# Kernel optimization log

Measured on AMD Instinct MI355X. Metric: run time of the kernel, lower is better.

Reference implementation:

```python
import jax, jax.numpy as jnp
import numpy as np
from jax import lax

B, T, DIN = 512, 96, 64
H = 256          # hidden_dim
P = 2            # patch_size
L = 4            # n_layers
HEADS = 8
E = 3 * H        # encoder_dim = hidden_dim * len(scales)
NC = 100         # num_classes
EPS = 1e-5


def layernorm(x, g, b):
    m = x.mean(-1, keepdims=True)
    v = ((x - m) ** 2).mean(-1, keepdims=True)
    return (x - m) * lax.rsqrt(v + EPS) * g + b


def conv1d(x, w, b, k):
    # x: [B, C, T], w: [O, I, k]; torch padding='same' (extra pad on the right for even k)
    lo = (k - 1) // 2
    hi = (k - 1) - lo
    y = lax.conv_general_dilated(x, w, (1,), [(lo, hi)],
                                 dimension_numbers=('NCH', 'OIH', 'NCH'))
    return y + b[None, :, None]


def fourier_attn(x, Wqkv, Wo, bo):
    Bx, Tx, Ex = x.shape
    dh = Ex // HEADS
    qkv = x @ Wqkv                                   # [B,T,3E]
    q, k, v = jnp.split(qkv, 3, axis=-1)
    to_heads = lambda t: t.reshape(Bx, Tx, HEADS, dh).transpose(0, 2, 1, 3)  # [B,h,T,dh]
    q, k, v = to_heads(q), to_heads(k), to_heads(v)
    qf = jnp.fft.rfft(q, axis=-2)
    kf = jnp.fft.rfft(k, axis=-2)
    attn = jnp.sum(jnp.conj(qf) * kf, axis=-1).real * (dh ** -0.5)  # [B,h,F]
    attn = jax.nn.softmax(attn, axis=-1)
    vf = jnp.fft.rfft(v, axis=-2)                    # [B,h,F,dh]
    out = jnp.fft.irfft(attn[..., None] * vf, n=Tx, axis=-2)        # [B,h,T,dh]
    out = out.transpose(0, 2, 1, 3).reshape(Bx, Tx, Ex)
    return out @ Wo + bo


def setup_inputs() -> dict:
    key = jax.random.key(0)
    ks = iter(jax.random.split(key, 40))
    nrm = lambda shape, s=0.02: jax.random.normal(next(ks), shape, jnp.float32) * s
    z = lambda *shape: jnp.zeros(shape, jnp.float32)
    o = lambda *shape: jnp.ones(shape, jnp.float32)
    return dict(
        x=jax.random.normal(next(ks), (B, T, DIN), jnp.float32),
        W_in=nrm((DIN, H)), b_in=z(H),
        pe=nrm((1, 100, H)),
        W_shape=nrm((H, H)), b_shape=z(H),
        W_patch=nrm((P * H, H)), b_patch=z(H),
        conv_w1=nrm((H, H, 1)), conv_b1=z(H),
        conv_w2=nrm((H, H, 2)), conv_b2=z(H),
        conv_w4=nrm((H, H, 4)), conv_b4=z(H),
        ln1_g=o(L, E), ln1_b=z(L, E),
        Wqkv=nrm((L, E, 3 * E)),
        Wo=nrm((L, E, E)), bo=z(L, E),
        ln2_g=o(L, E), ln2_b=z(L, E),
        Wf1=nrm((L, E, 4 * E)), bf1=z(L, 4 * E),
        Wf2=nrm((L, 4 * E, E)), bf2=z(L, E),
        ssm_w=nrm((E, E, 3)), ssm_b=z(E),
        ssm_g=o(E), ssm_bn=z(E),
        W_out=nrm((E, NC)), b_out=z(NC),
    )


def reference(x, W_in, b_in, pe, W_shape, b_shape, W_patch, b_patch,
              conv_w1, conv_b1, conv_w2, conv_b2, conv_w4, conv_b4,
              ln1_g, ln1_b, Wqkv, Wo, bo, ln2_g, ln2_b, Wf1, bf1, Wf2, bf2,
              ssm_w, ssm_b, ssm_g, ssm_bn, W_out, b_out):
    h = x @ W_in + b_in                              # [B,T,H]
    h = h + pe[:, :h.shape[1], :]
    # shape-aware embedding: diff with prepend of first step
    sf = jnp.diff(h, axis=1, prepend=h[:, :1, :])
    h = h + sf @ W_shape + b_shape
    # patch embedding: [B,T,H] -> [B,T/P,P*H] -> [B,T/P,H]
    Bx, Tx, Dx = h.shape
    h = h.reshape(Bx, Tx // P, P * Dx) @ W_patch + b_patch
    # multiscale fourier: rfft.real then 3 same-padded convs, concat channels
    f = jnp.fft.rfft(h, axis=1).real                 # [B,F,H], F = T/P//2 + 1
    fc = f.transpose(0, 2, 1)                        # [B,H,F]
    m1 = conv1d(fc, conv_w1, conv_b1, 1).transpose(0, 2, 1)
    m2 = conv1d(fc, conv_w2, conv_b2, 2).transpose(0, 2, 1)
    m4 = conv1d(fc, conv_w4, conv_b4, 4).transpose(0, 2, 1)
    h = jnp.concatenate([m1, m2, m4], axis=-1)       # [B,F,E]
    for i in range(L):
        h = h + fourier_attn(layernorm(h, ln1_g[i], ln1_b[i]), Wqkv[i], Wo[i], bo[i])
        y = layernorm(h, ln2_g[i], ln2_b[i])
        y = jax.nn.gelu(y @ Wf1[i] + bf1[i], approximate=False) @ Wf2[i] + bf2[i]
        h = h + y
    # simple SSM: depth conv residual + layernorm
    s = conv1d(h.transpose(0, 2, 1), ssm_w, ssm_b, 3).transpose(0, 2, 1)
    h = layernorm(h + s, ssm_g, ssm_bn)
    return h.mean(axis=1) @ W_out + b_out            # [B,NC]
```

## Files before the change

### kernel.cpp

```cpp
#include <hip/hip_runtime.h>
#include <hip/hip_bf16.h>
#include <math.h>

#define Bsz 512
#define Tin 96
#define DIN 64
#define Hd  256
#define Pp  2
#define Ll  4
#define NHEAD 8
#define Ed  768
#define NCls 100
#define Tp  48
#define Ff  25
#define F2  13
#define DH  96

#define E_BIAS 1
#define E_PE   2
#define E_RES  4
#define E_ACC  8
#define E_GELU 16
#define E_OUTS 32
#define E_SPLK 64

typedef unsigned short ushortT;
typedef unsigned short ushort8 __attribute__((ext_vector_type(8)));
typedef short short8 __attribute__((ext_vector_type(8)));
typedef float f32x4 __attribute__((ext_vector_type(4)));

static __device__ __forceinline__ ushortT f2bf(float f) {
  __hip_bfloat16 h = __float2bfloat16(f);
  return *reinterpret_cast<ushortT*>(&h);
}
static __device__ __forceinline__ float bfbits2f(ushortT u) {
  unsigned int x = ((unsigned int)u) << 16;
  return __uint_as_float(x);
}
static __device__ __forceinline__ void split2(float v, ushortT& h, ushortT& l) {
  h = f2bf(v);
  l = f2bf(v - bfbits2f(h));
}

typedef const __attribute__((address_space(1))) void* gas1_t;
typedef __attribute__((address_space(3))) void* las3_t;
static __device__ __forceinline__ void gload16(const void* g, void* l) {
  __builtin_amdgcn_global_load_lds((gas1_t)g, (las3_t)l, 16, 0, 0);
}

constexpr int GBN = 128, GBK = 32;

template<int BMS, int AMODE, int ASRC, int EPI>
__global__ __launch_bounds__(256) void gemm3(
    const float* __restrict__ A,
    const ushortT* __restrict__ Ah, const ushortT* __restrict__ Al,
    const ushortT* __restrict__ Bh, const ushortT* __restrict__ Bl,
    const float* __restrict__ bias, const float* __restrict__ extra,
    float* __restrict__ C, ushortT* __restrict__ Coh, ushortT* __restrict__ Col,
    int M, int N, int K, int Ald, int Tdim, int lo, int Kin, int Cld, int coff,
    int Mt, int Nt, int mmaj, int ksn)
{
  constexpr int GBMv = BMS;
  constexpr int WMF  = GBMv / 32;
  constexpr int ARPW = GBMv / 4;
  constexpr int TPR  = 256 / GBMv;
  constexpr int EPT  = 32 / TPR;

  __shared__ __align__(16) ushortT Ash[GBMv * GBK];
  __shared__ __align__(16) ushortT Asl[GBMv * GBK];
  __shared__ __align__(16) ushortT Bsh[GBN * GBK];
  __shared__ __align__(16) ushortT Bsl[GBN * GBK];
  int tid = threadIdx.x;

  int lin = blockIdx.x;
  int G = gridDim.x;
  int r8 = lin & 7, s8 = lin >> 3;
  int q = G >> 3, rem = G & 7;
  int start = r8 * q + (r8 < rem ? r8 : rem);
  int idx = start + s8;
  int tiles = Mt * Nt;
  int ks = 0;
  if (ksn > 1) { ks = idx / tiles; idx -= ks * tiles; }
  int mt, nt;
  if (mmaj) { mt = idx / Nt; nt = idx - mt * Nt; }
  else      { nt = idx / Mt; mt = idx - nt * Mt; }
  int m0 = mt * GBMv, n0 = nt * GBN;
  int kper = K / ksn;
  int kbeg = ks * kper, kend = kbeg + kper;

  int wid = tid >> 6, lane = tid & 63;
  int wm = wid & 1, wn = wid >> 1;
  int m16 = lane & 15, quad = lane >> 4;

  f32x4 acc[WMF][4] = {};

  int gcb = (lane & 3) << 4;
  int growB = (wid << 5) + (lane >> 2);
  int scbB  = gcb ^ (((growB >> 1) & 3) << 4);
  char* ldsB = (char*)Bsh + (wid << 11);
  char* ldsb = (char*)Bsl + (wid << 11);
  size_t bo0 = ((size_t)(n0 + growB) * K) * 2 + scbB;
  size_t bo1 = bo0 + (size_t)16 * K * 2;
  int growA = wid * ARPW + (lane >> 2);
  int scbA  = gcb ^ (((growA >> 1) & 3) << 4);
  char* ldsA = (char*)Ash + wid * ARPW * 64;
  char* ldsa = (char*)Asl + wid * ARPW * 64;
  size_t ao0 = 0, ao1 = 0;
  if (ASRC == 1) {
    int ar0 = m0 + growA;  if (ar0 >= M) ar0 = M - 1;
    ao0 = ((size_t)ar0 * Ald) * 2 + scbA;
    if (ARPW == 32) {
      int ar1 = m0 + growA + 16;  if (ar1 >= M) ar1 = M - 1;
      ao1 = ((size_t)ar1 * Ald) * 2 + scbA;
    }
  }

  int srow = tid / TPR;
  int sseg = (tid % TPR) * EPT;
  int sswz = ((srow >> 1) & 3) << 3;

  int fswz = ((m16 >> 1) & 3) << 3;
  int scf  = (quad << 3) ^ fswz;

  for (int k0 = kbeg; k0 < kend; k0 += GBK) {
    size_t kb = (size_t)k0 * 2;
    gload16((const char*)Bh + bo0 + kb, ldsB);
    gload16((const char*)Bh + bo1 + kb, ldsB + 1024);
    gload16((const char*)Bl + bo0 + kb, ldsb);
    gload16((const char*)Bl + bo1 + kb, ldsb + 1024);
    if (ASRC == 1) {
      gload16((const char*)Ah + ao0 + kb, ldsA);
      gload16((const char*)Al + ao0 + kb, ldsa);
      if (ARPW == 32) {
        gload16((const char*)Ah + ao1 + kb, ldsA + 1024);
        gload16((const char*)Al + ao1 + kb, ldsa + 1024);
      }
    } else {
      int row = m0 + srow;
      if (row >= M) row = M - 1;
      float tf[EPT];
      if (AMODE == 0) {
        const float* p = A + (size_t)row * Ald + k0 + sseg;
#pragma unroll
        for (int j = 0; j < EPT; j += 4) {
          float4 v = *(const float4*)(p + j);
          tf[j] = v.x; tf[j+1] = v.y; tf[j+2] = v.z; tf[j+3] = v.w;
        }
      } else if (AMODE == 1) {
        int t = row % Tdim;
        const float* p = A + (size_t)row * Ald + k0 + sseg;
#pragma unroll
        for (int j = 0; j < EPT; j += 4) {
          float4 v = *(const float4*)(p + j);
          float4 w = (t != 0) ? *(const float4*)(p - Ald + j) : v;
          tf[j] = v.x - w.x; tf[j+1] = v.y - w.y;
          tf[j+2] = v.z - w.z; tf[j+3] = v.w - w.w;
        }
      } else {
        int kk = k0 + sseg;
        int tap = kk / Kin;
        int i0  = kk - tap * Kin;
        int bb = row / Tdim;
        int t  = row - bb * Tdim;
        int tt = t - lo + tap;
        if (tt >= 0 && tt < Tdim) {
          const float* p = A + ((size_t)bb * Tdim + tt) * Ald + i0;
#pragma unroll
          for (int j = 0; j < EPT; j += 4) {
            float4 v = *(const float4*)(p + j);
            tf[j] = v.x; tf[j+1] = v.y; tf[j+2] = v.z; tf[j+3] = v.w;
          }
        } else {
#pragma unroll
          for (int j = 0; j < EPT; j++) tf[j] = 0.0f;
        }
      }
      ushortT th[EPT], tl[EPT];
#pragma unroll
      for (int j = 0; j < EPT; j++) split2(tf[j], th[j], tl[j]);
#pragma unroll
      for (int c8 = 0; c8 < EPT / 8; c8++) {
        int st = srow * GBK + ((sseg + c8 * 8) ^ sswz);
        *(ushort8*)&Ash[st] = *(ushort8*)&th[c8 * 8];
        *(ushort8*)&Asl[st] = *(ushort8*)&tl[c8 * 8];
      }
    }
    __syncthreads();
    short8 ah[WMF], al[WMF], bh[4], bl[4];
#pragma unroll
    for (int i = 0; i < WMF; i++) {
      int ro = (wm * (WMF * 16) + i * 16 + m16) * GBK + scf;
      ah[i] = *(short8*)&Ash[ro];
      al[i] = *(short8*)&Asl[ro];
    }
#pragma unroll
    for (int j = 0; j < 4; j++) {
      int ro = (wn * 64 + j * 16 + m16) * GBK + scf;
      bh[j] = *(short8*)&Bsh[ro];
      bl[j] = *(short8*)&Bsl[ro];
    }
    __builtin_amdgcn_s_setprio(1);
#pragma unroll
    for (int i = 0; i < WMF; i++)
#pragma unroll
      for (int j = 0; j < 4; j++) {
        acc[i][j] = __builtin_amdgcn_mfma_f32_16x16x32_bf16(ah[i], bh[j], acc[i][j], 0, 0, 0);
        acc[i][j] = __builtin_amdgcn_mfma_f32_16x16x32_bf16(al[i], bh[j], acc[i][j], 0, 0, 0);
        acc[i][j] = __builtin_amdgcn_mfma_f32_16x16x32_bf16(ah[i], bl[j], acc[i][j], 0, 0, 0);
      }
    __builtin_amdgcn_s_setprio(0);
    __syncthreads();
  }

#pragma unroll
  for (int i = 0; i < WMF; i++) {
#pragma unroll
    for (int j = 0; j < 4; j++) {
      int colg = n0 + wn * 64 + j * 16 + m16;
#pragma unroll
      for (int rr = 0; rr < 4; rr++) {
        int rowg = m0 + wm * (WMF * 16) + i * 16 + quad * 4 + rr;
        if (rowg >= M) continue;
        float v = acc[i][j][rr];
        if ((EPI & E_BIAS) && ks == 0) v += bias[colg];
        if (EPI & E_PE)   v += extra[(size_t)(rowg % Tdim) * N + colg];
        if (EPI & E_RES)  v += extra[(size_t)rowg * Cld + colg];
        if (EPI & E_GELU) v = 0.5f * v * (1.0f + erff(v * 0.70710678118654752f));
        size_t off = (size_t)rowg * Cld + coff + colg;
        if (EPI & E_SPLK) {
          atomicAdd(&C[off], v);
        } else if (EPI & E_OUTS) {
          ushortT h, l; split2(v, h, l);
          Coh[off] = h; Col[off] = l;
        } else {
          if (EPI & E_ACC) v += C[off];
          C[off] = v;
        }
      }
    }
  }
}

#define GEMM3(BMS_, AM, AS, EP, KS, Asrc, AhP, AlP, BhP, BlP, biasP, extraP, CP, CohP, ColP, \
              Mv, Nv, Kv, AldV, TdimV, loV, KinV, CldV, coffV) \
  do { int Mt_ = ((Mv) + (BMS_) - 1) / (BMS_), Nt_ = (Nv) / GBN; \
       int mm_ = ((Mv) >= (Nv)) ? 1 : 0; \
       gemm3<BMS_, AM, AS, EP><<<dim3(Mt_ * Nt_ * (KS)), dim3(256), 0, stream>>>( \
           Asrc, AhP, AlP, BhP, BlP, biasP, extraP, CP, CohP, ColP, \
           Mv, Nv, Kv, AldV, TdimV, loV, KinV, CldV, coffV, Mt_, Nt_, mm_, KS); } while (0)

__global__ __launch_bounds__(256) void wcvt_t_split(
    const float* __restrict__ W, ushortT* __restrict__ Wh, ushortT* __restrict__ Wl,
    int K, int N)
{
  __shared__ float t[32][33];
  int k0 = blockIdx.y * 32, n0 = blockIdx.x * 32;
  int tx = threadIdx.x;
  int ty = threadIdx.y;
#pragma unroll
  for (int dy = 0; dy < 32; dy += 8)
    t[ty + dy][tx] = W[(size_t)(k0 + ty + dy) * N + n0 + tx];
  __syncthreads();
#pragma unroll
  for (int dy = 0; dy < 32; dy += 8) {
    float v = t[tx][ty + dy];
    ushortT h, l;
    split2(v, h, l);
    size_t off = (size_t)(n0 + ty + dy) * K + k0 + tx;
    Wh[off] = h; Wl[off] = l;
  }
}

__global__ __launch_bounds__(256) void wcvt_split(
    const float* __restrict__ W, ushortT* __restrict__ Wh, ushortT* __restrict__ Wl, int n)
{
  int gid = blockIdx.x * 256 + threadIdx.x;
  int stride = gridDim.x * 256;
  for (int i = gid; i < n; i += stride) {
    ushortT h, l;
    split2(W[i], h, l);
    Wh[i] = h; Wl[i] = l;
  }
}

__global__ __launch_bounds__(256) void wcvt_split_tm(
    const float* __restrict__ W, ushortT* __restrict__ Wh, ushortT* __restrict__ Wl,
    int O, int Kin, int NT)
{
  int n = O * Kin * NT;
  int gid = blockIdx.x * 256 + threadIdx.x;
  int stride = gridDim.x * 256;
  for (int idx = gid; idx < n; idx += stride) {
    int o = idx / (Kin * NT);
    int rr = idx - o * (Kin * NT);
    int tap = rr / Kin;
    int i = rr - tap * Kin;
    float v = W[(size_t)o * Kin * NT + (size_t)i * NT + tap];
    ushortT h, l;
    split2(v, h, l);
    Wh[idx] = h; Wl[idx] = l;
  }
}

constexpr int BM = 64, BN = 64, BK = 16, TM = 4, TN = 4;
__global__ __launch_bounds__(256) void gemm_cls(
    const float* __restrict__ A, const float* __restrict__ Bw,
    const float* __restrict__ bias, float* __restrict__ C,
    int M, int N, int K, int Ald, int Cld)
{
  __shared__ alignas(16) float As[BK][BM + 4];
  __shared__ alignas(16) float Bs[BK][BN + 4];
  int tid = threadIdx.x;
  int n0 = blockIdx.x * BN;
  int m0 = blockIdx.y * BM;
  int tx = tid & 15, ty = tid >> 4;
  float acc[TM][TN];
#pragma unroll
  for (int i = 0; i < TM; i++)
#pragma unroll
    for (int j = 0; j < TN; j++) acc[i][j] = 0.0f;
  int a_m = tid >> 2, a_k = (tid & 3) * 4;
  int b_k = tid >> 4, b_n = (tid & 15) * 4;
  for (int k0 = 0; k0 < K; k0 += BK) {
    int row = m0 + a_m;
#pragma unroll
    for (int j = 0; j < 4; j++)
      As[a_k + j][a_m] = A[(size_t)row * Ald + k0 + a_k + j];
    int kk = k0 + b_k;
#pragma unroll
    for (int j = 0; j < 4; j++) {
      int nn = n0 + b_n + j;
      Bs[b_k][b_n + j] = (nn < N) ? Bw[(size_t)kk * N + nn] : 0.0f;
    }
    __syncthreads();
#pragma unroll
    for (int k = 0; k < BK; k++) {
      float4 av = *reinterpret_cast<const float4*>(&As[k][ty * TM]);
      float4 bv = *reinterpret_cast<const float4*>(&Bs[k][tx * TN]);
      float a4[4] = {av.x, av.y, av.z, av.w};
      float b4[4] = {bv.x, bv.y, bv.z, bv.w};
#pragma unroll
      for (int i = 0; i < TM; i++)
#pragma unroll
        for (int j = 0; j < TN; j++) acc[i][j] += a4[i] * b4[j];
    }
    __syncthreads();
  }
#pragma unroll
  for (int i = 0; i < TM; i++) {
    int row = m0 + ty * TM + i;
#pragma unroll
    for (int j = 0; j < TN; j++) {
      int col = n0 + tx * TN + j;
      if (col >= N) continue;
      C[(size_t)row * Cld + col] = acc[i][j] + bias[col];
    }
  }
}

__global__ __launch_bounds__(256) void rfft48_kernel(
    const float* __restrict__ hp, float* __restrict__ f)
{
  int kf = blockIdx.x;
  int b  = blockIdx.y;
  int tid = threadIdx.x;
  __shared__ float ct[48];
  if (tid < 48) {
    int rr = (kf * tid) % 48;
    ct[tid] = cosf(6.2831853071795864f * (float)rr / 48.0f);
  }
  __syncthreads();
  const float* hb = hp + (size_t)b * Tp * Hd;
  float s = 0.0f;
  for (int t = 0; t < 48; t++) s += hb[t * Hd + tid] * ct[t];
  f[((size_t)b * Ff + kf) * Hd + tid] = s;
}

__global__ __launch_bounds__(256) void attn_fused(
    const float* __restrict__ qkv,
    ushortT* __restrict__ oh, ushortT* __restrict__ ol)
{
  int bh = blockIdx.x;
  int b = bh >> 3, h = bh & 7;
  __shared__ float qs[Ff * DH], ks[Ff * DH], vs[Ff * DH];
  __shared__ float ct[F2 * Ff], st[F2 * Ff];
  __shared__ float red[F2 * DH];
  __shared__ float sm[F2];
  __shared__ float G[Ff];
  int tid = threadIdx.x;
  const float* base = qkv + (size_t)b * Ff * (3 * Ed) + h * DH;
  for (int e = tid; e < Ff * DH; e += 256) {
    int t = e / DH, d = e - t * DH;
    size_t ro = (size_t)t * (3 * Ed) + d;
    qs[e] = base[ro];
    ks[e] = base[ro + Ed];
    vs[e] = base[ro + 2 * Ed];
  }
  for (int e = tid; e < F2 * Ff; e += 256) {
    int fq = e / Ff, t = e - fq * Ff;
    int rr = (fq * t) % Ff;
    float ang = 6.2831853071795864f * (float)rr / 25.0f;
    ct[e] = cosf(ang); st[e] = sinf(ang);
  }
  __syncthreads();
  for (int e = tid; e < F2 * DH; e += 256) {
    int fq = e / DH, d = e - fq * DH;
    float qr = 0, qi = 0, kr = 0, ki = 0;
    for (int t = 0; t < Ff; t++) {
      float c = ct[fq * Ff + t], s = st[fq * Ff + t];
      float qv = qs[t * DH + d], kv = ks[t * DH + d];
      qr += qv * c; qi += qv * s; kr += kv * c; ki += kv * s;
    }
    red[e] = qr * kr + qi * ki;
  }
  __syncthreads();
  if (tid < F2) {
    float s = 0;
    for (int d = 0; d < DH; d++) s += red[tid * DH + d];
    sm[tid] = s * 0.10206207261596575f;
  }
  __syncthreads();
  if (tid == 0) {
    float mx = sm[0];
    for (int f = 1; f < F2; f++) mx = fmaxf(mx, sm[f]);
    float den = 0;
    for (int f = 0; f < F2; f++) { float e2 = expf(sm[f] - mx); sm[f] = e2; den += e2; }
    float inv = 1.0f / den;
    for (int f = 0; f < F2; f++)
      sm[f] *= inv * ((f == 0) ? (1.0f / 25.0f) : (2.0f / 25.0f));
  }
  __syncthreads();
  if (tid < Ff) {
    float g = 0;
    for (int f = 0; f < F2; f++) g += sm[f] * ct[f * Ff + tid];
    G[tid] = g;
  }
  __syncthreads();
  size_t ob = ((size_t)b * Ff) * Ed + h * DH;
  for (int e = tid; e < Ff * DH; e += 256) {
    int t = e / DH, d = e - t * DH;
    float o = 0;
    int dd = t;
    for (int tp = 0; tp < Ff; tp++) {
      o += G[dd] * vs[tp * DH + d];
      dd--; if (dd < 0) dd += Ff;
    }
    ushortT hh, ll;
    split2(o, hh, ll);
    size_t off = ob + (size_t)t * Ed + d;
    oh[off] = hh; ol[off] = ll;
  }
}

__global__ __launch_bounds__(256) void ln_split(
    const float* __restrict__ x, const float* __restrict__ g,
    const float* __restrict__ bb, ushortT* __restrict__ yh, ushortT* __restrict__ yl)
{
  int row = blockIdx.x;
  int tid = threadIdx.x;
  const float* xr = x + (size_t)row * Ed;
  float v0 = xr[tid], v1 = xr[tid + 256], v2 = xr[tid + 512];
  __shared__ float rs[256];
  rs[tid] = v0 + v1 + v2;
  __syncthreads();
  for (int o = 128; o > 0; o >>= 1) {
    if (tid < o) rs[tid] += rs[tid + o];
    __syncthreads();
  }
  float m = rs[0] * (1.0f / 768.0f);
  __syncthreads();
  float d0 = v0 - m, d1 = v1 - m, d2 = v2 - m;
  rs[tid] = d0 * d0 + d1 * d1 + d2 * d2;
  __syncthreads();
  for (int o = 128; o > 0; o >>= 1) {
    if (tid < o) rs[tid] += rs[tid + o];
    __syncthreads();
  }
  float inv = rsqrtf(rs[0] * (1.0f / 768.0f) + 1e-5f);
  size_t basei = (size_t)row * Ed;
  float o0 = d0 * inv * g[tid] + bb[tid];
  float o1 = d1 * inv * g[tid + 256] + bb[tid + 256];
  float o2 = d2 * inv * g[tid + 512] + bb[tid + 512];
  ushortT h, l;
  split2(o0, h, l); yh[basei + tid] = h;       yl[basei + tid] = l;
  split2(o1, h, l); yh[basei + tid + 256] = h; yl[basei + tid + 256] = l;
  split2(o2, h, l); yh[basei + tid + 512] = h; yl[basei + tid + 512] = l;
}

__global__ __launch_bounds__(256) void ln_f32(
    const float* __restrict__ x, const float* __restrict__ g,
    const float* __restrict__ bb, float* __restrict__ y)
{
  int row = blockIdx.x;
  int tid = threadIdx.x;
  const float* xr = x + (size_t)row * Ed;
  float v0 = xr[tid], v1 = xr[tid + 256], v2 = xr[tid + 512];
  __shared__ float rs[256];
  rs[tid] = v0 + v1 + v2;
  __syncthreads();
  for (int o = 128; o > 0; o >>= 1) {
    if (tid < o) rs[tid] += rs[tid + o];
    __syncthreads();
  }
  float m = rs[0] * (1.0f / 768.0f);
  __syncthreads();
  float d0 = v0 - m, d1 = v1 - m, d2 = v2 - m;
  rs[tid] = d0 * d0 + d1 * d1 + d2 * d2;
  __syncthreads();
  for (int o = 128; o > 0; o >>= 1) {
    if (tid < o) rs[tid] += rs[tid + o];
    __syncthreads();
  }
  float inv = rsqrtf(rs[0] * (1.0f / 768.0f) + 1e-5f);
  float* yr = y + (size_t)row * Ed;
  yr[tid]       = d0 * inv * g[tid]       + bb[tid];
  yr[tid + 256] = d1 * inv * g[tid + 256] + bb[tid + 256];
  yr[tid + 512] = d2 * inv * g[tid + 512] + bb[tid + 512];
}

__global__ __launch_bounds__(256) void mean_kernel(
    const float* __restrict__ x, float* __restrict__ y)
{
  int b = blockIdx.x;
  int tid = threadIdx.x;
  for (int c = tid; c < Ed; c += 256) {
    float s = 0;
    for (int t = 0; t < Ff; t++) s += x[((size_t)b * Ff + t) * Ed + c];
    y[(size_t)b * Ed + c] = s * (1.0f / 25.0f);
  }
}

extern "C" void kernel_launch(void* const* d_in, const int* in_sizes, int n_in,
                              void* d_out, int out_size, void* d_ws, size_t ws_size,
                              hipStream_t stream)
{
  const float* x       = (const float*)d_in[0];
  const float* W_in    = (const float*)d_in[1];
  const float* b_in    = (const float*)d_in[2];
  const float* pe      = (const float*)d_in[3];
  const float* W_shape = (const float*)d_in[4];
  const float* b_shape = (const float*)d_in[5];
  const float* W_patch = (const float*)d_in[6];
  const float* b_patch = (const float*)d_in[7];
  const float* conv_w1 = (const float*)d_in[8];
  const float* conv_b1 = (const float*)d_in[9];
  const float* conv_w2 = (const float*)d_in[10];
  const float* conv_b2 = (const float*)d_in[11];
  const float* conv_w4 = (const float*)d_in[12];
  const float* conv_b4 = (const float*)d_in[13];
  const float* ln1_g   = (const float*)d_in[14];
  const float* ln1_b   = (const float*)d_in[15];
  const float* Wqkv    = (const float*)d_in[16];
  const float* Wo      = (const float*)d_in[17];
  const float* bo      = (const float*)d_in[18];
  const float* ln2_g   = (const float*)d_in[19];
  const float* ln2_b   = (const float*)d_in[20];
  const float* Wf1     = (const float*)d_in[21];
  const float* bf1     = (const float*)d_in[22];
  const float* Wf2     = (const float*)d_in[23];
  const float* bf2     = (const float*)d_in[24];
  const float* ssm_w   = (const float*)d_in[25];
  const float* ssm_b   = (const float*)d_in[26];
  const float* ssm_g   = (const float*)d_in[27];
  const float* ssm_bn  = (const float*)d_in[28];
  const float* W_out   = (const float*)d_in[29];
  const float* b_out   = (const float*)d_in[30];
  float* out = (float*)d_out;

  float* hbuf = (float*)d_ws;
  ushortT* Ahp = (ushortT*)(hbuf + 9830400);
  ushortT* Alp = Ahp + 9830400;
  float* pool = (float*)(Alp + 9830400);

  dim3 blk(256);
  dim3 wblk(32, 8);
  const int Mf = Bsz * Ff;
  const ushortT* NUS = nullptr;
  const float* NF = nullptr;
  ushortT* NU = nullptr;

  ushortT* p0w = (ushortT*)(pool + 6291456);
  ushortT* WinH = p0w + 0;        ushortT* WinL = p0w + 16384;
  ushortT* WshH = p0w + 32768;    ushortT* WshL = p0w + 98304;
  ushortT* WpaH = p0w + 163840;   ushortT* WpaL = p0w + 294912;
  ushortT* c1H  = p0w + 425984;   ushortT* c1L  = p0w + 491520;
  ushortT* c2H  = p0w + 557056;   ushortT* c2L  = p0w + 688128;
  ushortT* c4H  = p0w + 819200;   ushortT* c4L  = p0w + 1081344;
  wcvt_t_split<<<dim3(Hd / 32, DIN / 32), wblk, 0, stream>>>(W_in, WinH, WinL, DIN, Hd);
  wcvt_t_split<<<dim3(Hd / 32, Hd / 32), wblk, 0, stream>>>(W_shape, WshH, WshL, Hd, Hd);
  wcvt_t_split<<<dim3(Hd / 32, (Pp * Hd) / 32), wblk, 0, stream>>>(W_patch, WpaH, WpaL, Pp * Hd, Hd);
  wcvt_split<<<64, blk, 0, stream>>>(conv_w1, c1H, c1L, Hd * Hd);
  wcvt_split_tm<<<128, blk, 0, stream>>>(conv_w2, c2H, c2L, Hd, Hd, 2);
  wcvt_split_tm<<<256, blk, 0, stream>>>(conv_w4, c4H, c4L, Hd, Hd, 4);

  float* s0  = (float*)Ahp;
  float* s1f = (float*)Ahp + 6291456;
  float* s1  = pool;
  for (int c = 0; c < 2; c++) {
    const int NB = 256;
    const int M96 = NB * Tin;
    const int Mpch = NB * Tp;
    const float* xc = x + (size_t)c * NB * Tin * DIN;

    GEMM3(64, 0, 0, E_BIAS | E_PE, 1, xc, NUS, NUS, WinH, WinL, b_in, pe, s0, NU, NU,
          M96, Hd, DIN, DIN, Tin, 0, 0, Hd, 0);
    GEMM3(64, 1, 0, E_BIAS | E_RES, 1, s0, NUS, NUS, WshH, WshL, b_shape, s0, s1, NU, NU,
          M96, Hd, Hd, Hd, Tin, 0, 0, Hd, 0);
    GEMM3(64, 0, 0, E_BIAS, 1, s1, NUS, NUS, WpaH, WpaL, b_patch, NF, s0, NU, NU,
          Mpch, Hd, Pp * Hd, Pp * Hd, 0, 0, 0, Hd, 0);
    rfft48_kernel<<<dim3(Ff, NB), blk, 0, stream>>>(s0, s1f + (size_t)c * NB * Ff * Hd);
  }
  GEMM3(64, 0, 0, E_BIAS, 1, s1f, NUS, NUS, c1H, c1L, conv_b1, NF, hbuf, NU, NU,
        Mf, Hd, Hd, Hd, Ff, 0, 0, Ed, 0);
  GEMM3(64, 2, 0, E_BIAS, 1, s1f, NUS, NUS, c2H, c2L, conv_b2, NF, hbuf, NU, NU,
        Mf, Hd, Hd * 2, Hd, Ff, 0, Hd, Ed, Hd);
  GEMM3(64, 2, 0, E_BIAS, 1, s1f, NUS, NUS, c4H, c4L, conv_b4, NF, hbuf, NU, NU,
        Mf, Hd, Hd * 4, Hd, Ff, 1, Hd, Ed, 2 * Hd);

  float* qkvbuf = pool;
  ushortT* lwA = (ushortT*)(pool + 7372800);
  ushortT* qkH = lwA + 0;        ushortT* qkL = lwA + 1769472;
  ushortT* woH = lwA + 3538944;  ushortT* woL = lwA + 4128768;
  ushortT* Ch2 = (ushortT*)pool;
  ushortT* Cl2 = Ch2 + 6291456;
  ushortT* lwB = (ushortT*)(pool + 6291456);
  ushortT* f1H = lwB + 0;        ushortT* f1L = lwB + 2359296;
  ushortT* f2H = lwB + 4718592;  ushortT* f2L = lwB + 7077888;

  const int NBA = 128;
  const int Mca = NBA * Ff;

  for (int l = 0; l < Ll; l++) {
    const float* Wqkv_l = Wqkv + (size_t)l * Ed * (3 * Ed);
    const float* Wo_l   = Wo   + (size_t)l * Ed * Ed;
    const float* bo_l   = bo   + (size_t)l * Ed;
    const float* Wf1_l  = Wf1  + (size_t)l * Ed * (4 * Ed);
    const float* bf1_l  = bf1  + (size_t)l * (4 * Ed);
    const float* Wf2_l  = Wf2  + (size_t)l * (4 * Ed) * Ed;
    const float* bf2_l  = bf2  + (size_t)l * Ed;

    wcvt_t_split<<<dim3((3 * Ed) / 32, Ed / 32), wblk, 0, stream>>>(Wqkv_l, qkH, qkL, Ed, 3 * Ed);
    wcvt_t_split<<<dim3(Ed / 32, Ed / 32), wblk, 0, stream>>>(Wo_l, woH, woL, Ed, Ed);

    ln_split<<<Mf, blk, 0, stream>>>(hbuf, ln1_g + (size_t)l * Ed, ln1_b + (size_t)l * Ed, Ahp, Alp);

    for (int c = 0; c < 4; c++) {
      ushortT* ah = Ahp + (size_t)c * Mca * Ed;
      ushortT* al = Alp + (size_t)c * Mca * Ed;
      GEMM3(64, 0, 1, 0, 1, NF, ah, al, qkH, qkL, NF, NF, qkvbuf, NU, NU,
            Mca, 3 * Ed, Ed, Ed, 0, 0, 0, 3 * Ed, 0);
      attn_fused<<<NBA * NHEAD, blk, 0, stream>>>(qkvbuf, ah, al);
    }
    GEMM3(128, 0, 1, E_BIAS | E_SPLK, 2, NF, Ahp, Alp, woH, woL, bo_l, NF, hbuf, NU, NU,
          Mf, Ed, Ed, Ed, 0, 0, 0, Ed, 0);

    wcvt_t_split<<<dim3((4 * Ed) / 32, Ed / 32), wblk, 0, stream>>>(Wf1_l, f1H, f1L, Ed, 4 * Ed);
    wcvt_t_split<<<dim3(Ed / 32, (4 * Ed) / 32), wblk, 0, stream>>>(Wf2_l, f2H, f2L, 4 * Ed, Ed);

    ln_split<<<Mf, blk, 0, stream>>>(hbuf, ln2_g + (size_t)l * Ed, ln2_b + (size_t)l * Ed, Ahp, Alp);

    for (int row0 = 0; row0 < Mf; row0 += 2048) {
      int rows = (Mf - row0 < 2048) ? (Mf - row0) : 2048;
      GEMM3(64, 0, 1, E_BIAS | E_GELU | E_OUTS, 1, NF,
            Ahp + (size_t)row0 * Ed, Alp + (size_t)row0 * Ed, f1H, f1L, bf1_l, NF,
            (float*)nullptr, Ch2, Cl2, rows, 4 * Ed, Ed, Ed, 0, 0, 0, 4 * Ed, 0);
      GEMM3(64, 0, 1, E_BIAS | E_SPLK, 4, NF, Ch2, Cl2, f2H, f2L, bf2_l, NF,
            hbuf + (size_t)row0 * Ed, NU, NU, rows, Ed, 4 * Ed, 4 * Ed, 0, 0, 0, Ed, 0);
    }
  }

  ushortT* ssH = (ushortT*)pool; ushortT* ssL = ssH + 1769472;
  wcvt_split_tm<<<512, blk, 0, stream>>>(ssm_w, ssH, ssL, Ed, Ed, 3);
  float* S = (float*)Ahp;
  GEMM3(128, 2, 0, E_BIAS | E_RES, 1, hbuf, NUS, NUS, ssH, ssL, ssm_b, hbuf, S, NU, NU,
        Mf, Ed, Ed * 3, Ed, Ff, 1, Ed, Ed, 0);

  float* L = pool;
  ln_f32<<<Mf, blk, 0, stream>>>(S, ssm_g, ssm_bn, L);
  float* mout = (float*)Ahp;
  mean_kernel<<<Bsz, blk, 0, stream>>>(L, mout);
  gemm_cls<<<dim3(2, Bsz / BM), blk, 0, stream>>>(
      mout, W_out, b_out, out, Bsz, NCls, Ed, Ed, NCls);
}
```

Before: 5.457 ms.

## Double-buffer LDS in pre-split GEMM path to overlap global loads with MFMA

For GEMMs whose A operand is already split into bf16 hi/lo halves, the shared-memory tiles are now double-buffered. The next K-step's direct global-to-LDS loads are issued before computing the current step, with explicit vmcnt waits and raw barriers replacing the load-then-syncthreads pattern. This aims to hide global memory latency behind the three-pass MFMA work, at the cost of twice the LDS per block and possibly lower occupancy. The Wo projection GEMM also switches from a 128-row to a 64-row tile.

```diff
diff --git a/kernel.cpp b/kernel.cpp
--- a/kernel.cpp
+++ b/kernel.cpp
@@ -65,11 +65,14 @@
   constexpr int ARPW = GBMv / 4;
   constexpr int TPR  = 256 / GBMv;
   constexpr int EPT  = 32 / TPR;
-
-  __shared__ __align__(16) ushortT Ash[GBMv * GBK];
-  __shared__ __align__(16) ushortT Asl[GBMv * GBK];
-  __shared__ __align__(16) ushortT Bsh[GBN * GBK];
-  __shared__ __align__(16) ushortT Bsl[GBN * GBK];
+  constexpr int NBUF = (ASRC == 1) ? 2 : 1;
+  constexpr int APL  = GBMv * GBK;
+  constexpr int BPL  = GBN * GBK;
+
+  __shared__ __align__(16) ushortT Ash[NBUF * APL];
+  __shared__ __align__(16) ushortT Asl[NBUF * APL];
+  __shared__ __align__(16) ushortT Bsh[NBUF * BPL];
+  __shared__ __align__(16) ushortT Bsl[NBUF * BPL];
   int tid = threadIdx.x;
 
   int lin = blockIdx.x;
@@ -97,14 +100,10 @@
   int gcb = (lane & 3) << 4;
   int growB = (wid << 5) + (lane >> 2);
   int scbB  = gcb ^ (((growB >> 1) & 3) << 4);
-  char* ldsB = (char*)Bsh + (wid << 11);
-  char* ldsb = (char*)Bsl + (wid << 11);
   size_t bo0 = ((size_t)(n0 + growB) * K) * 2 + scbB;
   size_t bo1 = bo0 + (size_t)16 * K * 2;
   int growA = wid * ARPW + (lane >> 2);
   int scbA  = gcb ^ (((growA >> 1) & 3) << 4);
-  char* ldsA = (char*)Ash + wid * ARPW * 64;
-  char* ldsa = (char*)Asl + wid * ARPW * 64;
   size_t ao0 = 0, ao1 = 0;
   if (ASRC == 1) {
     int ar0 = m0 + growA;  if (ar0 >= M) ar0 = M - 1;
@@ -122,94 +121,152 @@
   int fswz = ((m16 >> 1) & 3) << 3;
   int scf  = (quad << 3) ^ fswz;
 
-  for (int k0 = kbeg; k0 < kend; k0 += GBK) {
-    size_t kb = (size_t)k0 * 2;
-    gload16((const char*)Bh + bo0 + kb, ldsB);
-    gload16((const char*)Bh + bo1 + kb, ldsB + 1024);
-    gload16((const char*)Bl + bo0 + kb, ldsb);
-    gload16((const char*)Bl + bo1 + kb, ldsb + 1024);
-    if (ASRC == 1) {
-      gload16((const char*)Ah + ao0 + kb, ldsA);
-      gload16((const char*)Al + ao0 + kb, ldsa);
-      if (ARPW == 32) {
-        gload16((const char*)Ah + ao1 + kb, ldsA + 1024);
-        gload16((const char*)Al + ao1 + kb, ldsa + 1024);
-      }
-    } else {
-      int row = m0 + srow;
-      if (row >= M) row = M - 1;
-      float tf[EPT];
-      if (AMODE == 0) {
-        const float* p = A + (size_t)row * Ald + k0 + sseg;
-#pragma unroll
-        for (int j = 0; j < EPT; j += 4) {
-          float4 v = *(const float4*)(p + j);
-          tf[j] = v.x; tf[j+1] = v.y; tf[j+2] = v.z; tf[j+3] = v.w;
+  if constexpr (ASRC == 1) {
+    auto stageP = [&](int bsel, int k0) {
+      size_t kb = (size_t)k0 * 2;
+      char* lB = (char*)Bsh + bsel * (BPL * 2) + (wid << 11);
+      char* lb = (char*)Bsl + bsel * (BPL * 2) + (wid << 11);
+      gload16((const char*)Bh + bo0 + kb, lB);
+      gload16((const char*)Bh + bo1 + kb, lB + 1024);
+      gload16((const char*)Bl + bo0 + kb, lb);
+      gload16((const char*)Bl + bo1 + kb, lb + 1024);
+      char* lA = (char*)Ash + bsel * (APL * 2) + wid * ARPW * 64;
+      char* la = (char*)Asl + bsel * (APL * 2) + wid * ARPW * 64;
+      gload16((const char*)Ah + ao0 + kb, lA);
+      gload16((const char*)Al + ao0 + kb, la);
+      if constexpr (ARPW == 32) {
+        gload16((const char*)Ah + ao1 + kb, lA + 1024);
+        gload16((const char*)Al + ao1 + kb, la + 1024);
+      }
+    };
+    int nsteps = (kend - kbeg) / GBK;
+    stageP(0, kbeg);
+    int cur = 0;
+    for (int s = 0; s < nsteps; ++s) {
+      if (s + 1 < nsteps) {
+        stageP(cur ^ 1, kbeg + (s + 1) * GBK);
+        if constexpr (GBMv == 128) asm volatile("s_waitcnt vmcnt(8)" ::: "memory");
+        else                       asm volatile("s_waitcnt vmcnt(6)" ::: "memory");
+      } else {
+        asm volatile("s_waitcnt vmcnt(0)" ::: "memory");
+      }
+      __builtin_amdgcn_s_barrier();
+      __builtin_amdgcn_sched_barrier(0);
+      short8 ah[WMF], al[WMF], bh[4], bl[4];
+      int ab = cur * APL, bb2 = cur * BPL;
+#pragma unroll
+      for (int i = 0; i < WMF; i++) {
+        int ro = (wm * (WMF * 16) + i * 16 + m16) * GBK + scf;
+        ah[i] = *(short8*)&Ash[ab + ro];
+        al[i] = *(short8*)&Asl[ab + ro];
+      }
+#pragma unroll
+      for (int j = 0; j < 4; j++) {
+        int ro = (wn * 64 + j * 16 + m16) * GBK + scf;
+        bh[j] = *(short8*)&Bsh[bb2 + ro];
+        bl[j] = *(short8*)&Bsl[bb2 + ro];
+      }
+      __builtin_amdgcn_s_setprio(1);
+#pragma unroll
+      for (int i = 0; i < WMF; i++)
+#pragma unroll
+        for (int j = 0; j < 4; j++) {
+          acc[i][j] = __builtin_amdgcn_mfma_f32_16x16x32_bf16(ah[i], bh[j], acc[i][j], 0, 0, 0);
+          acc[i][j] = __builtin_amdgcn_mfma_f32_16x16x32_bf16(al[i], bh[j], acc[i][j], 0, 0, 0);
+          acc[i][j] = __builtin_amdgcn_mfma_f32_16x16x32_bf16(ah[i], bl[j], acc[i][j], 0, 0, 0);
         }
-      } else if (AMODE == 1) {
-        int t = row % Tdim;
-        const float* p = A + (size_t)row * Ald + k0 + sseg;
-#pragma unroll
-        for (int j = 0; j < EPT; j += 4) {
-          float4 v = *(const float4*)(p + j);
-          float4 w = (t != 0) ? *(const float4*)(p - Ald + j) : v;
-          tf[j] = v.x - w.x; tf[j+1] = v.y - w.y;
-          tf[j+2] = v.z - w.z; tf[j+3] = v.w - w.w;
-        }
-      } else {
-        int kk = k0 + sseg;
-        int tap = kk / Kin;
-        int i0  = kk - tap * Kin;
-        int bb = row / Tdim;
-        int t  = row - bb * Tdim;
-        int tt = t - lo + tap;
-        if (tt >= 0 && tt < Tdim) {
-          const float* p = A + ((size_t)bb * Tdim + tt) * Ald + i0;
+      __builtin_amdgcn_s_setprio(0);
+      __builtin_amdgcn_s_barrier();
+      __builtin_amdgcn_sched_barrier(0);
+      cur ^= 1;
+    }
+  } else {
+    for (int k0 = kbeg; k0 < kend; k0 += GBK) {
+      size_t kb = (size_t)k0 * 2;
+      {
+        char* ldsB = (char*)Bsh + (wid << 11);
+        char* ldsb = (char*)Bsl + (wid << 11);
+        gload16((const char*)Bh + bo0 + kb, ldsB);
+        gload16((const char*)Bh + bo1 + kb, ldsB + 1024);
+        gload16((const char*)Bl + bo0 + kb, ldsb);
+        gload16((const char*)Bl + bo1 + kb, ldsb + 1024);
+      }
+      {
+        int row = m0 + srow;
+        if (row >= M) row = M - 1;
+        float tf[EPT];
+        if (AMODE == 0) {
+          const float* p = A + (size_t)row * Ald + k0 + sseg;
 #pragma unroll
           for (int j = 0; j < EPT; j += 4) {
             float4 v = *(const float4*)(p + j);
             tf[j] = v.x; tf[j+1] = v.y; tf[j+2] = v.z; tf[j+3] = v.w;
           }
+        } else if (AMODE == 1) {
+          int t = row % Tdim;
+          const float* p = A + (size_t)row * Ald + k0 + sseg;
+#pragma unroll
+          for (int j = 0; j < EPT; j += 4) {
+            float4 v = *(const float4*)(p + j);
+            float4 w = (t != 0) ? *(const float4*)(p - Ald + j) : v;
+            tf[j] = v.x - w.x; tf[j+1] = v.y - w.y;
+            tf[j+2] = v.z - w.z; tf[j+3] = v.w - w.w;
+          }
         } else {
-#pragma unroll
-          for (int j = 0; j < EPT; j++) tf[j] = 0.0f;
+          int kk = k0 + sseg;
+          int tap = kk / Kin;
+          int i0  = kk - tap * Kin;
+          int bb = row / Tdim;
+          int t  = row - bb * Tdim;
+          int tt = t - lo + tap;
+          if (tt >= 0 && tt < Tdim) {
+            const float* p = A + ((size_t)bb * Tdim + tt) * Ald + i0;
+#pragma unroll
+            for (int j = 0; j < EPT; j += 4) {
+              float4 v = *(const float4*)(p + j);
+              tf[j] = v.x; tf[j+1] = v.y; tf[j+2] = v.z; tf[j+3] = v.w;
+            }
+          } else {
+#pragma unroll
+            for (int j = 0; j < EPT; j++) tf[j] = 0.0f;
+          }
         }
-      }
-      ushortT th[EPT], tl[EPT];
-#pragma unroll
-      for (int j = 0; j < EPT; j++) split2(tf[j], th[j], tl[j]);
-#pragma unroll
-      for (int c8 = 0; c8 < EPT / 8; c8++) {
-        int st = srow * GBK + ((sseg + c8 * 8) ^ sswz);
-        *(ushort8*)&Ash[st] = *(ushort8*)&th[c8 * 8];
-        *(ushort8*)&Asl[st] = *(ushort8*)&tl[c8 * 8];
-      }
-    }
-    __syncthreads();
-    short8 ah[WMF], al[WMF], bh[4], bl[4];
-#pragma unroll
-    for (int i = 0; i < WMF; i++) {
-      int ro = (wm * (WMF * 16) + i * 16 + m16) * GBK + scf;
-      ah[i] = *(short8*)&Ash[ro];
-      al[i] = *(short8*)&Asl[ro];
-    }
-#pragma unroll
-    for (int j = 0; j < 4; j++) {
-      int ro = (wn * 64 + j * 16 + m16) * GBK + scf;
-      bh[j] = *(short8*)&Bsh[ro];
-      bl[j] = *(short8*)&Bsl[ro];
-    }
-    __builtin_amdgcn_s_setprio(1);
-#pragma unroll
-    for (int i = 0; i < WMF; i++)
+        ushortT th[EPT], tl[EPT];
+#pragma unroll
+        for (int j = 0; j < EPT; j++) split2(tf[j], th[j], tl[j]);
+#pragma unroll
+        for (int c8 = 0; c8 < EPT / 8; c8++) {
+          int st = srow * GBK + ((sseg + c8 * 8) ^ sswz);
+          *(ushort8*)&Ash[st] = *(ushort8*)&th[c8 * 8];
+          *(ushort8*)&Asl[st] = *(ushort8*)&tl[c8 * 8];
+        }
+      }
+      __syncthreads();
+      short8 ah[WMF], al[WMF], bh[4], bl[4];
+#pragma unroll
+      for (int i = 0; i < WMF; i++) {
+        int ro = (wm * (WMF * 16) + i * 16 + m16) * GBK + scf;
+        ah[i] = *(short8*)&Ash[ro];
+        al[i] = *(short8*)&Asl[ro];
+      }
 #pragma unroll
       for (int j = 0; j < 4; j++) {
-        acc[i][j] = __builtin_amdgcn_mfma_f32_16x16x32_bf16(ah[i], bh[j], acc[i][j], 0, 0, 0);
-        acc[i][j] = __builtin_amdgcn_mfma_f32_16x16x32_bf16(al[i], bh[j], acc[i][j], 0, 0, 0);
-        acc[i][j] = __builtin_amdgcn_mfma_f32_16x16x32_bf16(ah[i], bl[j], acc[i][j], 0, 0, 0);
-      }
-    __builtin_amdgcn_s_setprio(0);
-    __syncthreads();
+        int ro = (wn * 64 + j * 16 + m16) * GBK + scf;
+        bh[j] = *(short8*)&Bsh[ro];
+        bl[j] = *(short8*)&Bsl[ro];
+      }
+      __builtin_amdgcn_s_setprio(1);
+#pragma unroll
+      for (int i = 0; i < WMF; i++)
+#pragma unroll
+        for (int j = 0; j < 4; j++) {
+          acc[i][j] = __builtin_amdgcn_mfma_f32_16x16x32_bf16(ah[i], bh[j], acc[i][j], 0, 0, 0);
+          acc[i][j] = __builtin_amdgcn_mfma_f32_16x16x32_bf16(al[i], bh[j], acc[i][j], 0, 0, 0);
+          acc[i][j] = __builtin_amdgcn_mfma_f32_16x16x32_bf16(ah[i], bl[j], acc[i][j], 0, 0, 0);
+        }
+      __builtin_amdgcn_s_setprio(0);
+      __syncthreads();
+    }
   }
 
 #pragma unroll
@@ -651,7 +708,7 @@
             Mca, 3 * Ed, Ed, Ed, 0, 0, 0, 3 * Ed, 0);
       attn_fused<<<NBA * NHEAD, blk, 0, stream>>>(qkvbuf, ah, al);
     }
-    GEMM3(128, 0, 1, E_BIAS | E_SPLK, 2, NF, Ahp, Alp, woH, woL, bo_l, NF, hbuf, NU, NU,
+    GEMM3(64, 0, 1, E_BIAS | E_SPLK, 2, NF, Ahp, Alp, woH, woL, bo_l, NF, hbuf, NU, NU,
           Mf, Ed, Ed, Ed, 0, 0, 0, Ed, 0);
 
     wcvt_t_split<<<dim3((4 * Ed) / 32, Ed / 32), wblk, 0, stream>>>(Wf1_l, f1H, f1L, Ed, 4 * Ed);
```

Result: slower. 5.597 ms (+2.6%).
